# Kernel tuning notes

Measured on AMD Instinct MI355X. Metric: run time of the kernel, lower is better.

## Reference

```python
import jax, jax.numpy as jnp
import numpy as np
from jax import lax

EPS = 1e-5
NUM_GROUPS = 32
OFFSET_SCALE = 1.0
K = 3            # deformable conv kernel size
KK = K * K
DWK = 7          # depthwise kernel size for offset predictor


def group_norm(x, gamma, beta, num_groups=NUM_GROUPS):
    B, C, H, W = x.shape
    xg = x.reshape(B, num_groups, C // num_groups, H, W)
    m = xg.mean(axis=(2, 3, 4), keepdims=True)
    v = xg.var(axis=(2, 3, 4), keepdims=True)
    xn = ((xg - m) * lax.rsqrt(v + EPS)).reshape(B, C, H, W)
    return xn * gamma[None, :, None, None] + beta[None, :, None, None]


def bilinear_gather(x, py, px):
    # x: [B,C,H,W]; py, px: [B,KK,H,W] absolute sample coords -> [B,C,KK,H,W]
    B, C, H, W = x.shape
    y0 = jnp.floor(py)
    x0 = jnp.floor(px)
    wy1 = py - y0
    wx1 = px - x0
    wy0 = 1.0 - wy1
    wx0 = 1.0 - wx1
    xf = x.reshape(B, C, H * W)

    def gather(yi, xi):
        valid = (yi >= 0) & (yi <= H - 1) & (xi >= 0) & (xi <= W - 1)
        yc = jnp.clip(yi, 0, H - 1).astype(jnp.int32)
        xc = jnp.clip(xi, 0, W - 1).astype(jnp.int32)
        idx = (yc * W + xc).reshape(B, -1)                      # [B, KK*H*W]
        g = jax.vmap(lambda a, i: a[:, i])(xf, idx)             # [B, C, KK*H*W]
        g = g.reshape(B, C, KK, H, W)
        return g * valid.astype(x.dtype)[:, None]

    out = (gather(y0, x0) * (wy0 * wx0)[:, None]
           + gather(y0, x0 + 1.0) * (wy0 * wx1)[:, None]
           + gather(y0 + 1.0, x0) * (wy1 * wx0)[:, None]
           + gather(y0 + 1.0, x0 + 1.0) * (wy1 * wx1)[:, None])
    return out


def deform_conv(x, dw, pw, pwb, w, b):
    # x: [B,C,H,W]; dw: [C,1,DWK,DWK] depthwise; pw: [2*KK,C,1,1]; w: [O,C,K,K]
    B, C, H, W = x.shape
    dn = ('NCHW', 'OIHW', 'NCHW')
    f = lax.conv_general_dilated(x, dw, (1, 1), 'SAME',
                                 feature_group_count=C, dimension_numbers=dn)
    off = lax.conv_general_dilated(f, pw, (1, 1), 'SAME', dimension_numbers=dn)
    off = (off + pwb[None, :, None, None]) * OFFSET_SCALE       # [B,2*KK,H,W]
    off = off.reshape(B, KK, 2, H, W)
    ks = jnp.arange(K, dtype=x.dtype) - (K - 1) / 2             # [-1,0,1]
    ky = jnp.repeat(ks, K)                                      # [KK]
    kx = jnp.tile(ks, K)
    yy, xx = jnp.meshgrid(jnp.arange(H, dtype=x.dtype),
                          jnp.arange(W, dtype=x.dtype), indexing='ij')
    py = yy[None, None] + ky[None, :, None, None] + off[:, :, 0]  # [B,KK,H,W]
    px = xx[None, None] + kx[None, :, None, None] + off[:, :, 1]
    sampled = bilinear_gather(x, py, px)                        # [B,C,KK,H,W]
    O = w.shape[0]
    out = jnp.einsum('bckhw,ock->bohw', sampled, w.reshape(O, C, KK))
    return out + b[None, :, None, None]


def setup_inputs() -> dict:
    key = jax.random.key(0)
    ks = jax.random.split(key, 10)
    B, C, H, W = 4, 256, 64, 64
    O = C
    x = jax.random.normal(ks[0], (B, C, H, W), dtype=jnp.float32)

    def conv_w(k, shape, fan_in):
        return jax.random.normal(k, shape, dtype=jnp.float32) / np.sqrt(fan_in)

    inp = {
        'x': x,
        'gn1_g': jnp.ones((C,), jnp.float32), 'gn1_b': jnp.zeros((C,), jnp.float32),
        'dw1': conv_w(ks[1], (C, 1, DWK, DWK), DWK * DWK),
        'pw1': jax.random.normal(ks[2], (2 * KK, C, 1, 1), jnp.float32) * 0.01,
        'pwb1': jnp.zeros((2 * KK,), jnp.float32),
        'w1': conv_w(ks[3], (O, C, K, K), C * KK),
        'b1': jnp.zeros((O,), jnp.float32),
        'gn2_g': jnp.ones((O,), jnp.float32), 'gn2_b': jnp.zeros((O,), jnp.float32),
        'dw2': conv_w(ks[4], (O, 1, DWK, DWK), DWK * DWK),
        'pw2': jax.random.normal(ks[5], (2 * KK, O, 1, 1), jnp.float32) * 0.01,
        'pwb2': jnp.zeros((2 * KK,), jnp.float32),
        'w2': conv_w(ks[6], (O, O, K, K), O * KK),
        'b2': jnp.zeros((O,), jnp.float32),
    }
    return inp


def reference(x, gn1_g, gn1_b, dw1, pw1, pwb1, w1, b1,
              gn2_g, gn2_b, dw2, pw2, pwb2, w2, b2):
    h = jax.nn.relu(group_norm(x, gn1_g, gn1_b))
    h = deform_conv(h, dw1, pw1, pwb1, w1, b1)
    h = jax.nn.relu(group_norm(h, gn2_g, gn2_b))
    # Dropout / DropPath are identity in eval mode
    h = deform_conv(h, dw2, pw2, pwb2, w2, b2)
    return h + x  # shortcut is Identity (in_channels == out_channels)
```

## Files before the change

kernel.cpp:

```cpp
#include <hip/hip_runtime.h>

#define B_    4
#define C_    256
#define H_    64
#define W_    64
#define HW_   4096
#define NG_   32
#define CPG_  8
#define KK_   9
#define NOFF_ 18

typedef __attribute__((ext_vector_type(8))) short short8;
typedef __attribute__((ext_vector_type(4))) short short4v;
typedef __attribute__((ext_vector_type(4))) float floatx4;
typedef __attribute__((ext_vector_type(16))) float floatx16;

static __device__ __forceinline__ short f2bf(float f) {
    union { float f; unsigned u; } v; v.f = f;
    unsigned r = v.u + 0x7fff + ((v.u >> 16) & 1);
    return (short)(r >> 16);
}
static __device__ __forceinline__ float bf2f(short s) {
    union { unsigned u; float f; } v;
    v.u = ((unsigned)(unsigned short)s) << 16;
    return v.f;
}
static __device__ __forceinline__ unsigned pkbf(float lo, float hi) {
    unsigned r;
    asm("v_cvt_pk_bf16_f32 %0, %1, %2" : "=v"(r) : "v"(lo), "v"(hi));
    return r;
}

__global__ __launch_bounds__(1024) void gn_relu_f32_kernel(
    const float* __restrict__ in, const float* __restrict__ gamma,
    const float* __restrict__ beta, short* __restrict__ outb)
{
    int b = blockIdx.x >> 5;
    int g = blockIdx.x & 31;
    const int N = CPG_ * HW_;
    size_t base = ((size_t)(b * C_ + g * CPG_)) * HW_;
    const float4* in4 = (const float4*)(in + base);
    int t = threadIdx.x;

    float s = 0.f, ss = 0.f;
    for (int i = t; i < N / 4; i += 1024) {
        float4 v = in4[i];
        s  += v.x + v.y + v.z + v.w;
        ss += v.x * v.x + v.y * v.y + v.z * v.z + v.w * v.w;
    }
    #pragma unroll
    for (int off = 32; off > 0; off >>= 1) {
        s  += __shfl_down(s, off, 64);
        ss += __shfl_down(ss, off, 64);
    }
    __shared__ float red[32];
    __shared__ float sh_rs, sh_m;
    int wid = t >> 6;
    if ((t & 63) == 0) { red[wid] = s; red[16 + wid] = ss; }
    __syncthreads();
    if (t == 0) {
        float S = 0.f, SS = 0.f;
        #pragma unroll
        for (int i = 0; i < 16; ++i) { S += red[i]; SS += red[16 + i]; }
        float m = S / (float)N;
        float var = SS / (float)N - m * m;
        sh_rs = rsqrtf(var + 1e-5f);
        sh_m = m;
    }
    __syncthreads();
    float rs = sh_rs, m = sh_m;
    short4v* out4 = (short4v*)(outb + base);
    for (int i = t; i < N / 4; i += 1024) {
        int ch = g * CPG_ + (i >> 10);
        float ga = gamma[ch] * rs;
        float be = beta[ch] - m * ga;
        float4 v = in4[i];
        short4v o;
        o.x = f2bf(fmaxf(fmaf(v.x, ga, be), 0.f));
        o.y = f2bf(fmaxf(fmaf(v.y, ga, be), 0.f));
        o.z = f2bf(fmaxf(fmaf(v.z, ga, be), 0.f));
        o.w = f2bf(fmaxf(fmaf(v.w, ga, be), 0.f));
        out4[i] = o;
    }
}

__global__ __launch_bounds__(1024) void gn_relu_bf16_kernel(
    const short* __restrict__ in, const float* __restrict__ gamma,
    const float* __restrict__ beta, short* __restrict__ outb)
{
    int b = blockIdx.x >> 5;
    int g = blockIdx.x & 31;
    const int N = CPG_ * HW_;
    size_t base = ((size_t)(b * C_ + g * CPG_)) * HW_;
    const short4v* in4 = (const short4v*)(in + base);
    int t = threadIdx.x;

    float s = 0.f, ss = 0.f;
    for (int i = t; i < N / 4; i += 1024) {
        short4v sv = in4[i];
        float vx = bf2f(sv.x), vy = bf2f(sv.y), vz = bf2f(sv.z), vw = bf2f(sv.w);
        s  += vx + vy + vz + vw;
        ss += vx * vx + vy * vy + vz * vz + vw * vw;
    }
    #pragma unroll
    for (int off = 32; off > 0; off >>= 1) {
        s  += __shfl_down(s, off, 64);
        ss += __shfl_down(ss, off, 64);
    }
    __shared__ float red[32];
    __shared__ float sh_rs, sh_m;
    int wid = t >> 6;
    if ((t & 63) == 0) { red[wid] = s; red[16 + wid] = ss; }
    __syncthreads();
    if (t == 0) {
        float S = 0.f, SS = 0.f;
        #pragma unroll
        for (int i = 0; i < 16; ++i) { S += red[i]; SS += red[16 + i]; }
        float m = S / (float)N;
        float var = SS / (float)N - m * m;
        sh_rs = rsqrtf(var + 1e-5f);
        sh_m = m;
    }
    __syncthreads();
    float rs = sh_rs, m = sh_m;
    short4v* out4 = (short4v*)(outb + base);
    for (int i = t; i < N / 4; i += 1024) {
        int ch = g * CPG_ + (i >> 10);
        float ga = gamma[ch] * rs;
        float be = beta[ch] - m * ga;
        short4v sv = in4[i];
        short4v o;
        o.x = f2bf(fmaxf(fmaf(bf2f(sv.x), ga, be), 0.f));
        o.y = f2bf(fmaxf(fmaf(bf2f(sv.y), ga, be), 0.f));
        o.z = f2bf(fmaxf(fmaf(bf2f(sv.z), ga, be), 0.f));
        o.w = f2bf(fmaxf(fmaf(bf2f(sv.w), ga, be), 0.f));
        out4[i] = o;
    }
}

__global__ __launch_bounds__(256) void dw7t_tr_kernel(
    const short* __restrict__ in,
    const float* __restrict__ dwk,
    short* __restrict__ fdwt,
    short* __restrict__ ht)
{
    __shared__ __align__(16) char smem[78112];
    int t = threadIdx.x;
    int blk = blockIdx.x;
    if (blk < 256) {
        short (*tile)[38][72] = (short(*)[38][72])smem;
        float (*wk8)[49]      = (float(*)[49])(smem + 43776);
        short (*outs)[2048]   = (short(*)[2048])(smem + 45344);
        int b = blk >> 6, o8 = (blk >> 1) & 31, rh = blk & 1;
        int c0 = o8 * 8;
        unsigned* tz = (unsigned*)smem;
        for (int i = t; i < 10944; i += 256) tz[i] = 0u;
        for (int i = t; i < 392; i += 256)
            wk8[i / 49][i % 49] = dwk[(c0 + i / 49) * 49 + (i % 49)];
        __syncthreads();
        for (int ch = 0; ch < 8; ++ch) {
            const short* src = in + ((size_t)(b * C_ + c0 + ch)) * HW_;
            for (int i = t; i < 608; i += 256) {
                int rr = i >> 4, xq = i & 15;
                int ry = rh * 32 + rr - 3;
                if (ry >= 0 && ry < 64) {
                    short4v v = *(const short4v*)(src + ry * 64 + xq * 4);
                    *(short4v*)&tile[ch][rr][4 + xq * 4] = v;
                }
            }
        }
        __syncthreads();
        for (int it = 0; it < 16; ++it) {
            int q = it * 256 + t;
            int ch = q >> 9, y = (q >> 4) & 31, x0 = (q & 15) << 2;
            float a0 = 0.f, a1 = 0.f, a2 = 0.f, a3 = 0.f;
            const float* wr0 = wk8[ch];
            #pragma unroll
            for (int dy = 0; dy < 7; ++dy) {
                const short* trw = &tile[ch][y + dy][x0];
                short4v s0 = *(const short4v*)trw;
                short4v s1 = *(const short4v*)(trw + 4);
                short4v s2 = *(const short4v*)(trw + 8);
                float r[12] = {bf2f(s0.x), bf2f(s0.y), bf2f(s0.z), bf2f(s0.w),
                               bf2f(s1.x), bf2f(s1.y), bf2f(s1.z), bf2f(s1.w),
                               bf2f(s2.x), bf2f(s2.y), bf2f(s2.z), bf2f(s2.w)};
                const float* wr = wr0 + dy * 7;
                #pragma unroll
                for (int dx = 0; dx < 7; ++dx) {
                    float wv = wr[dx];
                    a0 = fmaf(r[dx + 1], wv, a0);
                    a1 = fmaf(r[dx + 2], wv, a1);
                    a2 = fmaf(r[dx + 3], wv, a2);
                    a3 = fmaf(r[dx + 4], wv, a3);
                }
            }
            short4v o;
            o.x = f2bf(a0); o.y = f2bf(a1); o.z = f2bf(a2); o.w = f2bf(a3);
            *(short4v*)&outs[ch][y * 64 + x0] = o;
        }
        __syncthreads();
        for (int it = 0; it < 8; ++it) {
            int p = it * 256 + t;
            short8 v;
            #pragma unroll
            for (int ch = 0; ch < 8; ++ch) v[ch] = outs[ch][p];
            *(short8*)(fdwt + (((size_t)(b * 64 + rh * 32 + (p >> 6)) * 32 + o8) * 64
                               + (p & 63)) * 8) = v;
        }
    } else {
        unsigned* ltile = (unsigned*)smem;
        int q0 = blk - 256;
        int q = ((q0 & 7) << 5) | (q0 >> 3);
        int b = q >> 6;
        int px0 = (q & 63) * 64;
        const short* sb = in + (size_t)b * C_ * HW_;
        int pq4 = t & 15, cphi = t >> 4;
        #pragma unroll
        for (int i = 0; i < 8; ++i) {
            int cp = i * 16 + cphi;
            const short* r0 = sb + (size_t)(2 * cp) * HW_ + px0 + pq4 * 4;
            short4v lo = *(const short4v*)r0;
            short4v hi = *(const short4v*)(r0 + HW_);
            #pragma unroll
            for (int j = 0; j < 4; ++j) {
                int pl = pq4 * 4 + j;
                unsigned wrd = (unsigned)(unsigned short)lo[j]
                             | ((unsigned)(unsigned short)hi[j] << 16);
                ltile[pl * 132 + (cp ^ ((pl & 7) << 2))] = wrd;
            }
        }
        __syncthreads();
        int pl = t & 63, coq = t >> 6;
        #pragma unroll
        for (int r = 0; r < 8; ++r) {
            int co = r * 4 + coq;
            uint4 v = *(const uint4*)&ltile[pl * 132 + ((co * 4) ^ ((pl & 7) << 2))];
            *(uint4*)(ht + ((size_t)(b * 32 + co) * HW_ + px0 + pl) * 8) = v;
        }
    }
}

__global__ __launch_bounds__(256) void wpack_all_kernel(
    const float* __restrict__ w1, const float* __restrict__ w2,
    const float* __restrict__ pw1, const float* __restrict__ pw2,
    short* __restrict__ wp1, short* __restrict__ wp2,
    short* __restrict__ ppk1, short* __restrict__ ppk2)
{
    int blk = blockIdx.x;
    if (blk < 4608) {
        const float* w = (blk < 2304) ? w1 : w2;
        short* wp = (blk < 2304) ? wp1 : wp2;
        int idx = (blk % 2304) * 256 + threadIdx.x;
        int j    = idx & 7;
        int lane = (idx >> 3) & 63;
        int ot   = (idx >> 9) & 7;
        int slab = idx >> 12;
        int g = slab >> 4, cc16 = slab & 15;
        int o = ot * 32 + (lane & 31);
        int c = cc16 * 16 + (lane >> 5) * 8 + j;
        wp[idx] = f2bf(w[(size_t)(o * C_ + c) * KK_ + g]);
    } else {
        int q = blk - 4608;
        const float* pw = (q < 32) ? pw1 : pw2;
        short* ppk = (q < 32) ? ppk1 : ppk2;
        int idx = (q & 31) * 256 + threadIdx.x;
        int j = idx & 7, lane = (idx >> 3) & 63;
        int ot = (idx >> 9) & 1, sl = idx >> 10;
        int o = ot * 16 + (lane & 15);
        int k = sl * 32 + (lane >> 4) * 8 + j;
        ppk[idx] = (o < NOFF_) ? f2bf(pw[o * C_ + k]) : (short)0;
    }
}

__global__ __launch_bounds__(1024, 4) void deform_fused_kernel(
    const short* __restrict__ ht,   const short* __restrict__ fdw,
    const short* __restrict__ ppk,  const float* __restrict__ pwb,
    const short* __restrict__ wp,   const float* __restrict__ bias,
    const float* __restrict__ resid, float* __restrict__ outf,
    short* __restrict__ outb)
{
    int lb = ((blockIdx.x & 7) << 5) | (blockIdx.x >> 3);
    int b = lb >> 6;
    int row = lb & 63;
    __shared__ int   i00[576], i01[576], i10[576], i11[576];
    __shared__ float c00[576], c01[576], c10[576], c11[576];
    __shared__ __align__(16) short sbuf[2][2][8192];
    float* off_lds = (float*)&sbuf[0][0][0];
    int t = threadIdx.x;
    int wv = t >> 6, lane = t & 63;
    int pq = lane >> 4, pr = lane & 15;
    int l31 = lane & 31, hi = lane >> 5;

    if (wv < 8) {
        int ot = wv & 1, ptw = wv >> 1;
        int px = ptw * 16 + pr;
        const short8* fdw8 = (const short8*)fdw;
        size_t fbase = ((size_t)(b * 64 + row)) * 32;
        const short8* ap = (const short8*)ppk;
        floatx4 pacc = (floatx4){0.f, 0.f, 0.f, 0.f};
        #pragma unroll
        for (int sl = 0; sl < 8; ++sl) {
            short8 af = ap[(sl * 2 + ot) * 64 + lane];
            short8 bf = fdw8[(fbase + sl * 4 + pq) * 64 + px];
            pacc = __builtin_amdgcn_mfma_f32_16x16x32_bf16(af, bf, pacc, 0, 0, 0);
        }
        #pragma unroll
        for (int r = 0; r < 4; ++r) {
            int o = ot * 16 + pq * 4 + r;
            if (o < NOFF_) off_lds[o * 64 + px] = pacc[r] + pwb[o];
        }
    }
    __syncthreads();

    if (t < 576) {
        int e = t;
        int k = e >> 6, p = e & 63;
        float offy = off_lds[(2 * k) * 64 + p];
        float offx = off_lds[(2 * k + 1) * 64 + p];
        float py = (float)row + (float)(k / 3 - 1) + offy;
        float px = (float)p   + (float)(k % 3 - 1) + offx;
        float y0f = floorf(py), x0f = floorf(px);
        float wy1 = py - y0f, wx1 = px - x0f;
        float wy0 = 1.f - wy1, wx0 = 1.f - wx1;
        float y1f = y0f + 1.f, x1f = x0f + 1.f;
        bool vy0 = (y0f >= 0.f) && (y0f <= 63.f);
        bool vy1 = (y1f >= 0.f) && (y1f <= 63.f);
        bool vx0 = (x0f >= 0.f) && (x0f <= 63.f);
        bool vx1 = (x1f >= 0.f) && (x1f <= 63.f);
        int iy0 = (int)fminf(fmaxf(y0f, 0.f), 63.f);
        int iy1 = (int)fminf(fmaxf(y1f, 0.f), 63.f);
        int ix0 = (int)fminf(fmaxf(x0f, 0.f), 63.f);
        int ix1 = (int)fminf(fmaxf(x1f, 0.f), 63.f);
        i00[e] = iy0 * 64 + ix0; i01[e] = iy0 * 64 + ix1;
        i10[e] = iy1 * 64 + ix0; i11[e] = iy1 * 64 + ix1;
        c00[e] = (vy0 && vx0) ? wy0 * wx0 : 0.f;
        c01[e] = (vy0 && vx1) ? wy0 * wx1 : 0.f;
        c10[e] = (vy1 && vx0) ? wy1 * wx0 : 0.f;
        c11[e] = (vy1 && vx1) ? wy1 * wx1 : 0.f;
    }
    __syncthreads();

    int c8a = t & 7;
    int pan = (t >> 3) & 1;
    int spx = t >> 4;
    const short8* ht8 = (const short8*)ht;
    size_t gbase0 = ((size_t)(b * 32 + pan * 16 + c8a)) * HW_;
    size_t gbase1 = ((size_t)(b * 32 + pan * 16 + c8a + 8)) * HW_;
    int slotA = (c8a ^ (spx & 15)) * 8;
    int slotB = ((c8a + 8) ^ (spx & 15)) * 8;
    int srow = spx * 128;

    short8 ra[4], rb[4];
    auto prefetch = [&](int g) {
        int e = g * 64 + spx;
        int a00 = i00[e], a01 = i01[e], a10 = i10[e], a11 = i11[e];
        ra[0] = ht8[gbase0 + a00];
        ra[1] = ht8[gbase0 + a01];
        ra[2] = ht8[gbase0 + a10];
        ra[3] = ht8[gbase0 + a11];
        rb[0] = ht8[gbase1 + a00];
        rb[1] = ht8[gbase1 + a01];
        rb[2] = ht8[gbase1 + a10];
        rb[3] = ht8[gbase1 + a11];
    };
    auto stage_write = [&](int g, int bi) {
        int e = g * 64 + spx;
        float w00 = c00[e], w01 = c01[e], w10 = c10[e], w11 = c11[e];
        uint4 va, vb;
        float f0, f1;
        #define BLEND(R, J) (w00 * bf2f(R[0][J]) + w01 * bf2f(R[1][J]) \
                           + w10 * bf2f(R[2][J]) + w11 * bf2f(R[3][J]))
        f0 = BLEND(ra, 0); f1 = BLEND(ra, 1); va.x = pkbf(f0, f1);
        f0 = BLEND(ra, 2); f1 = BLEND(ra, 3); va.y = pkbf(f0, f1);
        f0 = BLEND(ra, 4); f1 = BLEND(ra, 5); va.z = pkbf(f0, f1);
        f0 = BLEND(ra, 6); f1 = BLEND(ra, 7); va.w = pkbf(f0, f1);
        f0 = BLEND(rb, 0); f1 = BLEND(rb, 1); vb.x = pkbf(f0, f1);
        f0 = BLEND(rb, 2); f1 = BLEND(rb, 3); vb.y = pkbf(f0, f1);
        f0 = BLEND(rb, 4); f1 = BLEND(rb, 5); vb.z = pkbf(f0, f1);
        f0 = BLEND(rb, 6); f1 = BLEND(rb, 7); vb.w = pkbf(f0, f1);
        #undef BLEND
        short* sp = &sbuf[bi][pan][srow];
        *(uint4*)&sp[slotA] = va;
        *(uint4*)&sp[slotB] = vb;
    };

    int pairId = wv & 7;
    int half = wv >> 3;

    floatx16 acc[2];
    #pragma unroll
    for (int i = 0; i < 16; ++i) { acc[0][i] = 0.f; acc[1][i] = 0.f; }

    prefetch(0);
    stage_write(0, 0);
    prefetch(1);
    __syncthreads();

    const short8* wp8 = (const short8*)wp;
    int msk = l31 & 15;

    for (int g = 0; g < 9; ++g) {
        const short* sb = &sbuf[g & 1][half][0];
        #pragma unroll
        for (int q4 = 0; q4 < 2; ++q4) {
            short8 af[4];
            #pragma unroll
            for (int qq = 0; qq < 4; ++qq)
                af[qq] = wp8[(size_t)(((g * 16 + half * 8 + q4 * 4 + qq) * 8 + pairId) * 64 + lane)];
            #pragma unroll
            for (int qq = 0; qq < 4; ++qq) {
                int ksl = q4 * 4 + qq;
                int so = ((((ksl << 1) | hi) ^ msk) << 3);
                short8 b0 = *(const short8*)&sb[l31 * 128 + so];
                short8 b1 = *(const short8*)&sb[(32 + l31) * 128 + so];
                acc[0] = __builtin_amdgcn_mfma_f32_32x32x16_bf16(af[qq], b0, acc[0], 0, 0, 0);
                acc[1] = __builtin_amdgcn_mfma_f32_32x32x16_bf16(af[qq], b1, acc[1], 0, 0, 0);
            }
        }
        if (g + 1 < 9) {
            stage_write(g + 1, (g + 1) & 1);
            if (g + 2 < 9) prefetch(g + 2);
        }
        __syncthreads();
    }

    float* xch = (float*)&sbuf[0][0][0];
    int wreg = (pairId * 2 + half) * 1024;
    floatx16 aw = half ? acc[0] : acc[1];
    floatx4* xq = (floatx4*)xch;
    #pragma unroll
    for (int j = 0; j < 4; ++j) {
        floatx4 v = {aw[j * 4 + 0], aw[j * 4 + 1], aw[j * 4 + 2], aw[j * 4 + 3]};
        xq[(wreg >> 2) + j * 64 + lane] = v;
    }
    __syncthreads();
    int rreg = (pairId * 2 + (half ^ 1)) * 1024;
    floatx16 ac = half ? acc[1] : acc[0];
    #pragma unroll
    for (int j = 0; j < 4; ++j) {
        floatx4 v = xq[(rreg >> 2) + j * 64 + lane];
        ac[j * 4 + 0] += v.x; ac[j * 4 + 1] += v.y;
        ac[j * 4 + 2] += v.z; ac[j * 4 + 3] += v.w;
    }

    #pragma unroll
    for (int r = 0; r < 16; ++r) {
        int o = pairId * 32 + (r & 3) + 8 * (r >> 2) + 4 * hi;
        float v = ac[r] + bias[o];
        size_t ob = ((size_t)(b * C_ + o)) * HW_ + row * 64 + half * 32 + l31;
        if (outf) {
            if (resid) v += resid[ob];
            outf[ob] = v;
        } else {
            outb[ob] = f2bf(v);
        }
    }
}

extern "C" void kernel_launch(void* const* d_in, const int* in_sizes, int n_in,
                              void* d_out, int out_size, void* d_ws, size_t ws_size,
                              hipStream_t stream)
{
    const float* x     = (const float*)d_in[0];
    const float* gn1_g = (const float*)d_in[1];
    const float* gn1_b = (const float*)d_in[2];
    const float* dw1   = (const float*)d_in[3];
    const float* pw1   = (const float*)d_in[4];
    const float* pwb1  = (const float*)d_in[5];
    const float* w1    = (const float*)d_in[6];
    const float* b1    = (const float*)d_in[7];
    const float* gn2_g = (const float*)d_in[8];
    const float* gn2_b = (const float*)d_in[9];
    const float* dw2   = (const float*)d_in[10];
    const float* pw2   = (const float*)d_in[11];
    const float* pwb2  = (const float*)d_in[12];
    const float* w2    = (const float*)d_in[13];
    const float* b2    = (const float*)d_in[14];
    float* out = (float*)d_out;

    float* ws   = (float*)d_ws;
    short* y1b  = (short*)ws;
    short* hbf  = (short*)(ws + 2097152);
    short* hbt  = (short*)(ws + 4194304);
    short* fdwt = (short*)(ws + 8388608);
    short* wp1  = (short*)(ws + 10485760);
    short* wp2  = (short*)(ws + 10780672);
    short* ppk1 = (short*)(ws + 11075584);
    short* ppk2 = (short*)(ws + 11079680);

    wpack_all_kernel<<<4672, 256, 0, stream>>>(w1, w2, pw1, pw2,
                                               wp1, wp2, ppk1, ppk2);

    gn_relu_f32_kernel<<<B_ * NG_, 1024, 0, stream>>>(x, gn1_g, gn1_b, hbf);
    dw7t_tr_kernel<<<512, 256, 0, stream>>>(hbf, dw1, fdwt, hbt);
    deform_fused_kernel<<<B_ * H_, 1024, 0, stream>>>(
        hbt, fdwt, ppk1, pwb1, wp1, b1, nullptr, nullptr, y1b);

    gn_relu_bf16_kernel<<<B_ * NG_, 1024, 0, stream>>>(y1b, gn2_g, gn2_b, hbf);
    dw7t_tr_kernel<<<512, 256, 0, stream>>>(hbf, dw2, fdwt, hbt);
    deform_fused_kernel<<<B_ * H_, 1024, 0, stream>>>(
        hbt, fdwt, ppk2, pwb2, wp2, b2, x, out, nullptr);
}
```

Measured before the change: 288.0 us.

## Use channel-last activations and split deform conv blocks into half-row tiles

```diff
diff --git a/kernel.cpp b/kernel.cpp
--- a/kernel.cpp
+++ b/kernel.cpp
@@ -230,12 +230,12 @@
             }
         }
         __syncthreads();
-        int pl = t & 63, coq = t >> 6;
+        int co = t & 31, ph2 = t >> 5;
         #pragma unroll
         for (int r = 0; r < 8; ++r) {
-            int co = r * 4 + coq;
+            int pl = r * 8 + ph2;
             uint4 v = *(const uint4*)&ltile[pl * 132 + ((co * 4) ^ ((pl & 7) << 2))];
-            *(uint4*)(ht + ((size_t)(b * 32 + co) * HW_ + px0 + pl) * 8) = v;
+            *(uint4*)(ht + ((size_t)b * HW_ + px0 + pl) * C_ + co * 8) = v;
         }
     }
 }
@@ -272,28 +272,30 @@
     }
 }
 
-__global__ __launch_bounds__(1024, 4) void deform_fused_kernel(
+__global__ __launch_bounds__(512, 4) void deform_fused_kernel(
     const short* __restrict__ ht,   const short* __restrict__ fdw,
     const short* __restrict__ ppk,  const float* __restrict__ pwb,
     const short* __restrict__ wp,   const float* __restrict__ bias,
     const float* __restrict__ resid, float* __restrict__ outf,
     short* __restrict__ outb)
 {
-    int lb = ((blockIdx.x & 7) << 5) | (blockIdx.x >> 3);
-    int b = lb >> 6;
-    int row = lb & 63;
-    __shared__ int   i00[576], i01[576], i10[576], i11[576];
-    __shared__ float c00[576], c01[576], c10[576], c11[576];
-    __shared__ __align__(16) short sbuf[2][2][8192];
-    float* off_lds = (float*)&sbuf[0][0][0];
+    int lb = ((blockIdx.x & 7) << 6) | (blockIdx.x >> 3);
+    int b = lb >> 7;
+    int row = (lb >> 1) & 63;
+    int ph = lb & 1;
+    __shared__ int   i00[288], i01[288], i10[288], i11[288];
+    __shared__ float c00[288], c01[288], c10[288], c11[288];
+    __shared__ __align__(16) short sbuf[2][8192];
+    float* off_lds = (float*)&sbuf[0][0];
     int t = threadIdx.x;
     int wv = t >> 6, lane = t & 63;
     int pq = lane >> 4, pr = lane & 15;
     int l31 = lane & 31, hi = lane >> 5;
 
-    if (wv < 8) {
+    if (wv < 4) {
         int ot = wv & 1, ptw = wv >> 1;
-        int px = ptw * 16 + pr;
+        int pxl = ptw * 16 + pr;
+        int px = ph * 32 + pxl;
         const short8* fdw8 = (const short8*)fdw;
         size_t fbase = ((size_t)(b * 64 + row)) * 32;
         const short8* ap = (const short8*)ppk;
@@ -307,18 +309,17 @@
         #pragma unroll
         for (int r = 0; r < 4; ++r) {
             int o = ot * 16 + pq * 4 + r;
-            if (o < NOFF_) off_lds[o * 64 + px] = pacc[r] + pwb[o];
-        }
-    }
-    __syncthreads();
-
-    if (t < 576) {
-        int e = t;
-        int k = e >> 6, p = e & 63;
-        float offy = off_lds[(2 * k) * 64 + p];
-        float offx = off_lds[(2 * k + 1) * 64 + p];
+            if (o < NOFF_) off_lds[o * 32 + pxl] = pacc[r] + pwb[o];
+        }
+    }
+    __syncthreads();
+
+    if (t < 288) {
+        int k = t >> 5, p = t & 31;
+        float offy = off_lds[(2 * k) * 32 + p];
+        float offx = off_lds[(2 * k + 1) * 32 + p];
         float py = (float)row + (float)(k / 3 - 1) + offy;
-        float px = (float)p   + (float)(k % 3 - 1) + offx;
+        float px = (float)(ph * 32 + p) + (float)(k % 3 - 1) + offx;
         float y0f = floorf(py), x0f = floorf(px);
         float wy1 = py - y0f, wx1 = px - x0f;
         float wy0 = 1.f - wy1, wx0 = 1.f - wx1;
@@ -331,40 +332,41 @@
         int iy1 = (int)fminf(fmaxf(y1f, 0.f), 63.f);
         int ix0 = (int)fminf(fmaxf(x0f, 0.f), 63.f);
         int ix1 = (int)fminf(fmaxf(x1f, 0.f), 63.f);
-        i00[e] = iy0 * 64 + ix0; i01[e] = iy0 * 64 + ix1;
-        i10[e] = iy1 * 64 + ix0; i11[e] = iy1 * 64 + ix1;
-        c00[e] = (vy0 && vx0) ? wy0 * wx0 : 0.f;
-        c01[e] = (vy0 && vx1) ? wy0 * wx1 : 0.f;
-        c10[e] = (vy1 && vx0) ? wy1 * wx0 : 0.f;
-        c11[e] = (vy1 && vx1) ? wy1 * wx1 : 0.f;
+        i00[t] = iy0 * 64 + ix0; i01[t] = iy0 * 64 + ix1;
+        i10[t] = iy1 * 64 + ix0; i11[t] = iy1 * 64 + ix1;
+        c00[t] = (vy0 && vx0) ? wy0 * wx0 : 0.f;
+        c01[t] = (vy0 && vx1) ? wy0 * wx1 : 0.f;
+        c10[t] = (vy1 && vx0) ? wy1 * wx0 : 0.f;
+        c11[t] = (vy1 && vx1) ? wy1 * wx1 : 0.f;
     }
     __syncthreads();
 
     int c8a = t & 7;
     int pan = (t >> 3) & 1;
     int spx = t >> 4;
-    const short8* ht8 = (const short8*)ht;
-    size_t gbase0 = ((size_t)(b * 32 + pan * 16 + c8a)) * HW_;
-    size_t gbase1 = ((size_t)(b * 32 + pan * 16 + c8a + 8)) * HW_;
-    int slotA = (c8a ^ (spx & 15)) * 8;
-    int slotB = ((c8a + 8) ^ (spx & 15)) * 8;
-    int srow = spx * 128;
+    const short* hb0 = ht + ((size_t)b * HW_) * C_ + pan * 128 + c8a * 8;
+    const short* hb1 = hb0 + 64;
+    int oct0 = pan * 16 + c8a;
+    int oct1 = oct0 + 8;
+    int slotA = ((oct0 & 16) | ((oct0 ^ spx) & 15)) * 8;
+    int slotB = ((oct1 & 16) | ((oct1 ^ spx) & 15)) * 8;
+    int srow = spx * 256;
 
     short8 ra[4], rb[4];
     auto prefetch = [&](int g) {
-        int e = g * 64 + spx;
+        int e = g * 32 + spx;
         int a00 = i00[e], a01 = i01[e], a10 = i10[e], a11 = i11[e];
-        ra[0] = ht8[gbase0 + a00];
-        ra[1] = ht8[gbase0 + a01];
-        ra[2] = ht8[gbase0 + a10];
-        ra[3] = ht8[gbase0 + a11];
-        rb[0] = ht8[gbase1 + a00];
-        rb[1] = ht8[gbase1 + a01];
-        rb[2] = ht8[gbase1 + a10];
-        rb[3] = ht8[gbase1 + a11];
+        ra[0] = *(const short8*)(hb0 + (size_t)a00 * C_);
+        ra[1] = *(const short8*)(hb0 + (size_t)a01 * C_);
+        ra[2] = *(const short8*)(hb0 + (size_t)a10 * C_);
+        ra[3] = *(const short8*)(hb0 + (size_t)a11 * C_);
+        rb[0] = *(const short8*)(hb1 + (size_t)a00 * C_);
+        rb[1] = *(const short8*)(hb1 + (size_t)a01 * C_);
+        rb[2] = *(const short8*)(hb1 + (size_t)a10 * C_);
+        rb[3] = *(const short8*)(hb1 + (size_t)a11 * C_);
     };
     auto stage_write = [&](int g, int bi) {
-        int e = g * 64 + spx;
+        int e = g * 32 + spx;
         float w00 = c00[e], w01 = c01[e], w10 = c10[e], w11 = c11[e];
         uint4 va, vb;
         float f0, f1;
@@ -379,17 +381,16 @@
         f0 = BLEND(rb, 4); f1 = BLEND(rb, 5); vb.z = pkbf(f0, f1);
         f0 = BLEND(rb, 6); f1 = BLEND(rb, 7); vb.w = pkbf(f0, f1);
         #undef BLEND
-        short* sp = &sbuf[bi][pan][srow];
+        short* sp = &sbuf[bi][srow];
         *(uint4*)&sp[slotA] = va;
         *(uint4*)&sp[slotB] = vb;
     };
 
-    int pairId = wv & 7;
-    int half = wv >> 3;
-
-    floatx16 acc[2];
+    int pairId = wv;
+
+    floatx16 acc;
     #pragma unroll
-    for (int i = 0; i < 16; ++i) { acc[0][i] = 0.f; acc[1][i] = 0.f; }
+    for (int i = 0; i < 16; ++i) acc[i] = 0.f;
 
     prefetch(0);
     stage_write(0, 0);
@@ -397,24 +398,22 @@
     __syncthreads();
 
     const short8* wp8 = (const short8*)wp;
-    int msk = l31 & 15;
 
     for (int g = 0; g < 9; ++g) {
-        const short* sb = &sbuf[g & 1][half][0];
-        #pragma unroll
-        for (int q4 = 0; q4 < 2; ++q4) {
+        const short* sb = &sbuf[g & 1][0];
+        #pragma unroll
+        for (int q4 = 0; q4 < 4; ++q4) {
             short8 af[4];
             #pragma unroll
             for (int qq = 0; qq < 4; ++qq)
-                af[qq] = wp8[(size_t)(((g * 16 + half * 8 + q4 * 4 + qq) * 8 + pairId) * 64 + lane)];
+                af[qq] = wp8[(size_t)(((g * 16 + q4 * 4 + qq) * 8 + pairId) * 64 + lane)];
             #pragma unroll
             for (int qq = 0; qq < 4; ++qq) {
-                int ksl = q4 * 4 + qq;
-                int so = ((((ksl << 1) | hi) ^ msk) << 3);
-                short8 b0 = *(const short8*)&sb[l31 * 128 + so];
-                short8 b1 = *(const short8*)&sb[(32 + l31) * 128 + so];
-                acc[0] = __builtin_amdgcn_mfma_f32_32x32x16_bf16(af[qq], b0, acc[0], 0, 0, 0);
-                acc[1] = __builtin_amdgcn_mfma_f32_32x32x16_bf16(af[qq], b1, acc[1], 0, 0, 0);
+                int s = q4 * 4 + qq;
+                int oct = s * 2 + hi;
+                int so = ((oct & 16) | ((oct ^ l31) & 15)) << 3;
+                short8 b0 = *(const short8*)&sb[l31 * 256 + so];
+                acc = __builtin_amdgcn_mfma_f32_32x32x16_bf16(af[qq], b0, acc, 0, 0, 0);
             }
         }
         if (g + 1 < 9) {
@@ -424,30 +423,11 @@
         __syncthreads();
     }
 
-    float* xch = (float*)&sbuf[0][0][0];
-    int wreg = (pairId * 2 + half) * 1024;
-    floatx16 aw = half ? acc[0] : acc[1];
-    floatx4* xq = (floatx4*)xch;
-    #pragma unroll
-    for (int j = 0; j < 4; ++j) {
-        floatx4 v = {aw[j * 4 + 0], aw[j * 4 + 1], aw[j * 4 + 2], aw[j * 4 + 3]};
-        xq[(wreg >> 2) + j * 64 + lane] = v;
-    }
-    __syncthreads();
-    int rreg = (pairId * 2 + (half ^ 1)) * 1024;
-    floatx16 ac = half ? acc[1] : acc[0];
-    #pragma unroll
-    for (int j = 0; j < 4; ++j) {
-        floatx4 v = xq[(rreg >> 2) + j * 64 + lane];
-        ac[j * 4 + 0] += v.x; ac[j * 4 + 1] += v.y;
-        ac[j * 4 + 2] += v.z; ac[j * 4 + 3] += v.w;
-    }
-
     #pragma unroll
     for (int r = 0; r < 16; ++r) {
         int o = pairId * 32 + (r & 3) + 8 * (r >> 2) + 4 * hi;
-        float v = ac[r] + bias[o];
-        size_t ob = ((size_t)(b * C_ + o)) * HW_ + row * 64 + half * 32 + l31;
+        float v = acc[r] + bias[o];
+        size_t ob = ((size_t)(b * C_ + o)) * HW_ + row * 64 + ph * 32 + l31;
         if (outf) {
             if (resid) v += resid[ob];
             outf[ob] = v;
@@ -493,11 +473,11 @@
 
     gn_relu_f32_kernel<<<B_ * NG_, 1024, 0, stream>>>(x, gn1_g, gn1_b, hbf);
     dw7t_tr_kernel<<<512, 256, 0, stream>>>(hbf, dw1, fdwt, hbt);
-    deform_fused_kernel<<<B_ * H_, 1024, 0, stream>>>(
+    deform_fused_kernel<<<512, 512, 0, stream>>>(
         hbt, fdwt, ppk1, pwb1, wp1, b1, nullptr, nullptr, y1b);
 
     gn_relu_bf16_kernel<<<B_ * NG_, 1024, 0, stream>>>(y1b, gn2_g, gn2_b, hbf);
     dw7t_tr_kernel<<<512, 256, 0, stream>>>(hbf, dw2, fdwt, hbt);
-    deform_fused_kernel<<<B_ * H_, 1024, 0, stream>>>(
+    deform_fused_kernel<<<512, 512, 0, stream>>>(
         hbt, fdwt, ppk2, pwb2, wp2, b2, x, out, nullptr);
 }
```

New measurement: 256.1 us. 11.1% less time.

## Store activations channel-last per pixel and batch weight fragment loads

Applied to the files above, without the earlier changes.

```diff
diff --git a/kernel.cpp b/kernel.cpp
--- a/kernel.cpp
+++ b/kernel.cpp
@@ -230,12 +230,12 @@
             }
         }
         __syncthreads();
-        int pl = t & 63, coq = t >> 6;
+        int co = t & 31, ph2 = t >> 5;
         #pragma unroll
         for (int r = 0; r < 8; ++r) {
-            int co = r * 4 + coq;
+            int pl = r * 8 + ph2;
             uint4 v = *(const uint4*)&ltile[pl * 132 + ((co * 4) ^ ((pl & 7) << 2))];
-            *(uint4*)(ht + ((size_t)(b * 32 + co) * HW_ + px0 + pl) * 8) = v;
+            *(uint4*)(ht + ((size_t)b * HW_ + px0 + pl) * C_ + co * 8) = v;
         }
     }
 }
@@ -250,15 +250,17 @@
     if (blk < 4608) {
         const float* w = (blk < 2304) ? w1 : w2;
         short* wp = (blk < 2304) ? wp1 : wp2;
-        int idx = (blk % 2304) * 256 + threadIdx.x;
-        int j    = idx & 7;
-        int lane = (idx >> 3) & 63;
-        int ot   = (idx >> 9) & 7;
-        int slab = idx >> 12;
-        int g = slab >> 4, cc16 = slab & 15;
-        int o = ot * 32 + (lane & 31);
-        int c = cc16 * 16 + (lane >> 5) * 8 + j;
-        wp[idx] = f2bf(w[(size_t)(o * C_ + c) * KK_ + g]);
+        int src = (blk % 2304) * 256 + threadIdx.x;
+        float v = w[src];
+        int o = src / (C_ * KK_);
+        int r = src - o * (C_ * KK_);
+        int c = r / KK_;
+        int g = r - c * KK_;
+        int ot   = o >> 5;
+        int lane = (o & 31) | (((c >> 3) & 1) << 5);
+        int j    = c & 7;
+        int slab = g * 16 + (c >> 4);
+        wp[(slab << 12) | (ot << 9) | (lane << 3) | j] = f2bf(v);
     } else {
         int q = blk - 4608;
         const float* pw = (q < 32) ? pw1 : pw2;
@@ -343,9 +345,8 @@
     int c8a = t & 7;
     int pan = (t >> 3) & 1;
     int spx = t >> 4;
-    const short8* ht8 = (const short8*)ht;
-    size_t gbase0 = ((size_t)(b * 32 + pan * 16 + c8a)) * HW_;
-    size_t gbase1 = ((size_t)(b * 32 + pan * 16 + c8a + 8)) * HW_;
+    const short* hb0 = ht + ((size_t)b * HW_) * C_ + pan * 128 + c8a * 8;
+    const short* hb1 = hb0 + 64;
     int slotA = (c8a ^ (spx & 15)) * 8;
     int slotB = ((c8a + 8) ^ (spx & 15)) * 8;
     int srow = spx * 128;
@@ -354,14 +355,14 @@
     auto prefetch = [&](int g) {
         int e = g * 64 + spx;
         int a00 = i00[e], a01 = i01[e], a10 = i10[e], a11 = i11[e];
-        ra[0] = ht8[gbase0 + a00];
-        ra[1] = ht8[gbase0 + a01];
-        ra[2] = ht8[gbase0 + a10];
-        ra[3] = ht8[gbase0 + a11];
-        rb[0] = ht8[gbase1 + a00];
-        rb[1] = ht8[gbase1 + a01];
-        rb[2] = ht8[gbase1 + a10];
-        rb[3] = ht8[gbase1 + a11];
+        ra[0] = *(const short8*)(hb0 + (size_t)a00 * C_);
+        ra[1] = *(const short8*)(hb0 + (size_t)a01 * C_);
+        ra[2] = *(const short8*)(hb0 + (size_t)a10 * C_);
+        ra[3] = *(const short8*)(hb0 + (size_t)a11 * C_);
+        rb[0] = *(const short8*)(hb1 + (size_t)a00 * C_);
+        rb[1] = *(const short8*)(hb1 + (size_t)a01 * C_);
+        rb[2] = *(const short8*)(hb1 + (size_t)a10 * C_);
+        rb[3] = *(const short8*)(hb1 + (size_t)a11 * C_);
     };
     auto stage_write = [&](int g, int bi) {
         int e = g * 64 + spx;
@@ -401,21 +402,17 @@
 
     for (int g = 0; g < 9; ++g) {
         const short* sb = &sbuf[g & 1][half][0];
-        #pragma unroll
-        for (int q4 = 0; q4 < 2; ++q4) {
-            short8 af[4];
-            #pragma unroll
-            for (int qq = 0; qq < 4; ++qq)
-                af[qq] = wp8[(size_t)(((g * 16 + half * 8 + q4 * 4 + qq) * 8 + pairId) * 64 + lane)];
-            #pragma unroll
-            for (int qq = 0; qq < 4; ++qq) {
-                int ksl = q4 * 4 + qq;
-                int so = ((((ksl << 1) | hi) ^ msk) << 3);
-                short8 b0 = *(const short8*)&sb[l31 * 128 + so];
-                short8 b1 = *(const short8*)&sb[(32 + l31) * 128 + so];
-                acc[0] = __builtin_amdgcn_mfma_f32_32x32x16_bf16(af[qq], b0, acc[0], 0, 0, 0);
-                acc[1] = __builtin_amdgcn_mfma_f32_32x32x16_bf16(af[qq], b1, acc[1], 0, 0, 0);
-            }
+        short8 af[8];
+        #pragma unroll
+        for (int q = 0; q < 8; ++q)
+            af[q] = wp8[(size_t)(((g * 16 + half * 8 + q) * 8 + pairId) * 64 + lane)];
+        #pragma unroll
+        for (int q = 0; q < 8; ++q) {
+            int so = ((((q << 1) | hi) ^ msk) << 3);
+            short8 b0 = *(const short8*)&sb[l31 * 128 + so];
+            short8 b1 = *(const short8*)&sb[(32 + l31) * 128 + so];
+            acc[0] = __builtin_amdgcn_mfma_f32_32x32x16_bf16(af[q], b0, acc[0], 0, 0, 0);
+            acc[1] = __builtin_amdgcn_mfma_f32_32x32x16_bf16(af[q], b1, acc[1], 0, 0, 0);
         }
         if (g + 1 < 9) {
             stage_write(g + 1, (g + 1) & 1);
```

New measurement: 269.6 us. 6.4% less time.
